# Optimization experiments

Measured on AMD Instinct MI355X. Metric: run time of the kernel, lower is better.

The kernel has to match this reference:

```python
import jax, jax.numpy as jnp
import numpy as np

B, S, D, H = 2, 1024, 2048, 16
NOPE, ROPE, VD, KVR, QLR = 128, 64, 128, 512, 1536
NE, TOPK, MI, SMI = 16, 2, 1408, 2816
QKD = NOPE + ROPE
SCALE = QKD ** -0.5
EPS = 1e-3


def _rms(x, w):
    return w * (x * jax.lax.rsqrt(jnp.mean(x * x, axis=-1, keepdims=True) + EPS))


def _lin(x, w, b):
    return x @ w.T + b


def _rope(x, cos, sin):
    # x: (B,S,H,dr); cos/sin: (S, dr//2); consecutive-pair complex rotation as in torch view_as_complex
    xs = x.reshape(*x.shape[:-1], -1, 2)
    x0, x1 = xs[..., 0], xs[..., 1]
    c = cos[None, :, None, :]
    s = sin[None, :, None, :]
    y = jnp.stack([x0 * c - x1 * s, x0 * s + x1 * c], axis=-1)
    return y.reshape(x.shape)


def setup_inputs() -> dict:
    ks = iter(jax.random.split(jax.random.key(0), 64))

    def w(*shape):
        return jax.random.normal(next(ks), shape, jnp.float32) * 0.02

    ang = jnp.arange(S)[:, None] * (1.0 / (10000.0 ** (jnp.arange(0, ROPE, 2) / ROPE)))[None, :]
    return {
        "x": jax.random.normal(next(ks), (B, S, D), jnp.float32),
        "attn_norm_w": jnp.ones(D, jnp.float32),
        "ffn_norm_w": jnp.ones(D, jnp.float32),
        "wq_a_w": w(QLR, D), "wq_a_b": w(QLR),
        "q_norm_w": jnp.ones(QLR, jnp.float32),
        "wq_b_w": w(H * QKD, QLR), "wq_b_b": w(H * QKD),
        "wkv_a_w": w(KVR + ROPE, D), "wkv_a_b": w(KVR + ROPE),
        "kv_norm_w": jnp.ones(KVR, jnp.float32),
        "wkv_b_w": w(H * (NOPE + VD), KVR),
        "wo_w": w(D, H * VD), "wo_b": w(D),
        "gate_w": w(NE, D), "gate_b": w(NE),
        "e_w1": w(NE, MI, D), "e_b1": w(NE, MI),
        "e_w2": w(NE, D, MI), "e_b2": w(NE, D),
        "e_w3": w(NE, MI, D), "e_b3": w(NE, MI),
        "s_w1": w(SMI, D), "s_b1": w(SMI),
        "s_w2": w(D, SMI), "s_b2": w(D),
        "s_w3": w(SMI, D), "s_b3": w(SMI),
        "cos": jnp.cos(ang), "sin": jnp.sin(ang),
        "start_pos": 0,
    }


def _forward(x, attn_norm_w, ffn_norm_w, wq_a_w, wq_a_b, q_norm_w, wq_b_w, wq_b_b,
             wkv_a_w, wkv_a_b, kv_norm_w, wkv_b_w, wo_w, wo_b,
             gate_w, gate_b, e_w1, e_b1, e_w2, e_b2, e_w3, e_b3,
             s_w1, s_b1, s_w2, s_b2, s_w3, s_b3, cos, sin, start_pos):
    # ---------------- MLA attention ----------------
    h = _rms(x, attn_norm_w)
    q = _lin(_rms(_lin(h, wq_a_w, wq_a_b), q_norm_w), wq_b_w, wq_b_b).reshape(B, S, H, QKD)
    q_nope, q_pe = q[..., :NOPE], q[..., NOPE:]
    q_pe = _rope(q_pe, cos, sin)
    kvf = _lin(h, wkv_a_w, wkv_a_b)
    kv, k_pe = kvf[..., :KVR], kvf[..., KVR:]
    k_pe = _rope(k_pe[:, :, None, :], cos, sin)[:, :, 0, :]          # (B,S,ROPE)
    wb = wkv_b_w.reshape(H, NOPE + VD, KVR)
    q_abs = jnp.einsum('bshd,hdc->bshc', q_nope, wb[:, :NOPE])       # absorbed q (B,S,H,KVR)
    kv_n = _rms(kv, kv_norm_w)                                       # kv cache content, start_pos=0
    scores = (jnp.einsum('bshc,btc->bsht', q_abs, kv_n)
              + jnp.einsum('bshr,btr->bsht', q_pe, k_pe)) * SCALE
    # NOTE: source constructs a causal mask but never applies it -> full attention (faithful)
    p = jax.nn.softmax(scores.astype(jnp.float32), axis=-1).astype(x.dtype)
    o = jnp.einsum('bsht,btc->bshc', p, kv_n)
    o = jnp.einsum('bshc,hdc->bshd', o, wb[:, NOPE:])
    x = x + _lin(o.reshape(B, S, H * VD), wo_w, wo_b)
    # ---------------- MoE FFN ----------------
    h2 = _rms(x, ffn_norm_w).reshape(-1, D)                          # (T,D)
    probs = jax.nn.softmax((h2 @ gate_w.T + gate_b).astype(jnp.float32), axis=-1)
    _, idx = jax.lax.top_k(probs + gate_b, TOPK)                     # bias re-added post-softmax, as in source
    wts = jnp.take_along_axis(probs, idx, axis=-1).astype(x.dtype)   # route_scale = 1.0
    T = h2.shape[0]
    combine = jnp.zeros((T, NE), x.dtype).at[jnp.arange(T)[:, None], idx].add(wts)
    a = jnp.einsum('td,eid->tei', h2, e_w1) + e_b1
    g = jax.nn.silu(a) * (jnp.einsum('td,eid->tei', h2, e_w3) + e_b3)
    gm = g * combine[:, :, None]
    y = jnp.einsum('tei,edi->td', gm, e_w2) + combine @ e_b2
    z = _lin(jax.nn.silu(_lin(h2, s_w1, s_b1)) * _lin(h2, s_w3, s_b3), s_w2, s_b2)
    return x + (y + z + h2).reshape(B, S, D)


def reference(x, attn_norm_w, ffn_norm_w, wq_a_w, wq_a_b, q_norm_w, wq_b_w, wq_b_b,
              wkv_a_w, wkv_a_b, kv_norm_w, wkv_b_w, wo_w, wo_b,
              gate_w, gate_b, e_w1, e_b1, e_w2, e_b2, e_w3, e_b3,
              s_w1, s_b1, s_w2, s_b2, s_w3, s_b3, cos, sin, start_pos):
    return _forward(x, attn_norm_w, ffn_norm_w, wq_a_w, wq_a_b, q_norm_w, wq_b_w, wq_b_b,
                    wkv_a_w, wkv_a_b, kv_norm_w, wkv_b_w, wo_w, wo_b,
                    gate_w, gate_b, e_w1, e_b1, e_w2, e_b2, e_w3, e_b3,
                    s_w1, s_b1, s_w2, s_b2, s_w3, s_b3, cos, sin, start_pos)
```

## Files before the change

kernel.cpp:

```cpp
#include <hip/hip_runtime.h>
#include <math.h>

constexpr int B_ = 2, S_ = 1024, D_ = 2048, H_ = 16;
constexpr int NOPE_ = 128, ROPE_ = 64, VD_ = 128, KVR_ = 512, QLR_ = 1536;
constexpr int NE_ = 16, MI_ = 1408, SMI_ = 2816;
constexpr int QKD_ = NOPE_ + ROPE_;
constexpr int T_ = B_ * S_;
constexpr float SCALE_ = 0.07216878364870322f;
constexpr float EPS_ = 1e-3f;
constexpr int MAX_TILES_ = 80;

typedef __attribute__((ext_vector_type(8))) short  bf16x8_t;
typedef __attribute__((ext_vector_type(4))) float  f32x4_t;
typedef __attribute__((ext_vector_type(4))) unsigned short us4_t;

__device__ __forceinline__ void split_bf(float v, unsigned short& h, unsigned short& l)
{
    unsigned int u = __float_as_uint(v);
    h = (unsigned short)(u >> 16);
    float lo = v - __uint_as_float(u & 0xFFFF0000u);
    l = (unsigned short)(__float_as_uint(lo) >> 16);
}

__device__ __forceinline__ void split4(const float4& v, us4_t& h, us4_t& l)
{
    split_bf(v.x, ((unsigned short*)&h)[0], ((unsigned short*)&l)[0]);
    split_bf(v.y, ((unsigned short*)&h)[1], ((unsigned short*)&l)[1]);
    split_bf(v.z, ((unsigned short*)&h)[2], ((unsigned short*)&l)[2]);
    split_bf(v.w, ((unsigned short*)&h)[3], ((unsigned short*)&l)[3]);
}

__device__ __forceinline__ void stage_rows(
    const float* __restrict__ P, int ldp, int row0, int rowclamp,
    int kt, int sr, int scol,
    unsigned short (*__restrict__ Hs)[40], unsigned short (*__restrict__ Ls)[40])
{
    #pragma unroll
    for (int rr = 0; rr < 128; rr += 32) {
        int row = row0 + rr + sr;
        if (row > rowclamp) row = rowclamp;
        const float4 v = *(const float4*)(P + (long)row * ldp + (kt + scol));
        us4_t h, l;
        split4(v, h, l);
        *(us4_t*)&Hs[rr + sr][scol] = h;
        *(us4_t*)&Ls[rr + sr][scol] = l;
    }
}

__global__ __launch_bounds__(256) void gemm_mfma_kernel(
    const float* __restrict__ A, int lda, long strideA,
    const float* __restrict__ W, int ldw, long strideW, int w_kn,
    const float* __restrict__ A2, int lda2, long strideA2,
    const float* __restrict__ W2, int ldw2, long strideW2, int K2,
    const float* __restrict__ bias, long strideBias,
    const float* __restrict__ res, int ldr, long strideRes, int res_mode,
    float* __restrict__ C, int ldc, long strideC,
    int Nlim, int K)
{
    const int bz = blockIdx.z;
    A += (long)bz * strideA;
    W += (long)bz * strideW;
    C += (long)bz * strideC;
    if (A2)   A2  += (long)bz * strideA2;
    if (W2)   W2  += (long)bz * strideW2;
    if (bias) bias += (long)bz * strideBias;
    if (res)  res  += (long)bz * strideRes;

    __shared__ unsigned short Ah[128][40], Al[128][40];
    __shared__ unsigned short Bh[128][40], Bl[128][40];

    const int m0 = blockIdx.y * 128;
    const int n0 = blockIdx.x * 128;
    const int tid  = threadIdx.x;
    const int lane = tid & 63;
    const int wv   = tid >> 6;
    const int wm = (wv >> 1) * 64, wn = (wv & 1) * 64;
    const int r16 = lane & 15, g4 = lane >> 4;

    f32x4_t acc[4][4];
    #pragma unroll
    for (int i = 0; i < 4; i++)
        #pragma unroll
        for (int j = 0; j < 4; j++) acc[i][j] = (f32x4_t){0.f, 0.f, 0.f, 0.f};

    const int sr   = tid >> 3;
    const int scol = (tid & 7) * 4;
    const int tcol = tid & 63, tkr = tid >> 6;

    for (int kt = 0; kt < K; kt += 32) {
        stage_rows(A, lda, m0, 1 << 30, kt, sr, scol, Ah, Al);
        if (w_kn == 0) {
            stage_rows(W, ldw, n0, Nlim - 1, kt, sr, scol, Bh, Bl);
        } else {
            #pragma unroll
            for (int cb = 0; cb < 128; cb += 64)
                #pragma unroll
                for (int kb = 0; kb < 32; kb += 4) {
                    float v = W[(long)(kt + kb + tkr) * ldw + (n0 + cb + tcol)];
                    unsigned short h, l;
                    split_bf(v, h, l);
                    Bh[cb + tcol][kb + tkr] = h;
                    Bl[cb + tcol][kb + tkr] = l;
                }
        }
        __syncthreads();

        bf16x8_t ah[4], al[4], bh[4], bl[4];
        #pragma unroll
        for (int i = 0; i < 4; i++) {
            ah[i] = *(const bf16x8_t*)&Ah[wm + i * 16 + r16][g4 * 8];
            al[i] = *(const bf16x8_t*)&Al[wm + i * 16 + r16][g4 * 8];
            bh[i] = *(const bf16x8_t*)&Bh[wn + i * 16 + r16][g4 * 8];
            bl[i] = *(const bf16x8_t*)&Bl[wn + i * 16 + r16][g4 * 8];
        }
        #pragma unroll
        for (int i = 0; i < 4; i++)
            #pragma unroll
            for (int j = 0; j < 4; j++) {
                f32x4_t t = acc[i][j];
                t = __builtin_amdgcn_mfma_f32_16x16x32_bf16(ah[i], bh[j], t, 0, 0, 0);
                t = __builtin_amdgcn_mfma_f32_16x16x32_bf16(ah[i], bl[j], t, 0, 0, 0);
                t = __builtin_amdgcn_mfma_f32_16x16x32_bf16(al[i], bh[j], t, 0, 0, 0);
                acc[i][j] = t;
            }
        __syncthreads();
    }

    if (K2 > 0) {
        for (int kt = 0; kt < K2; kt += 32) {
            stage_rows(A2, lda2, m0, 1 << 30, kt, sr, scol, Ah, Al);
            stage_rows(W2, ldw2, n0, Nlim - 1, kt, sr, scol, Bh, Bl);
            __syncthreads();
            bf16x8_t ah[4], al[4], bh[4], bl[4];
            #pragma unroll
            for (int i = 0; i < 4; i++) {
                ah[i] = *(const bf16x8_t*)&Ah[wm + i * 16 + r16][g4 * 8];
                al[i] = *(const bf16x8_t*)&Al[wm + i * 16 + r16][g4 * 8];
                bh[i] = *(const bf16x8_t*)&Bh[wn + i * 16 + r16][g4 * 8];
                bl[i] = *(const bf16x8_t*)&Bl[wn + i * 16 + r16][g4 * 8];
            }
            #pragma unroll
            for (int i = 0; i < 4; i++)
                #pragma unroll
                for (int j = 0; j < 4; j++) {
                    f32x4_t t = acc[i][j];
                    t = __builtin_amdgcn_mfma_f32_16x16x32_bf16(ah[i], bh[j], t, 0, 0, 0);
                    t = __builtin_amdgcn_mfma_f32_16x16x32_bf16(ah[i], bl[j], t, 0, 0, 0);
                    t = __builtin_amdgcn_mfma_f32_16x16x32_bf16(al[i], bh[j], t, 0, 0, 0);
                    acc[i][j] = t;
                }
            __syncthreads();
        }
    }

    #pragma unroll
    for (int i = 0; i < 4; i++)
        #pragma unroll
        for (int rr = 0; rr < 4; rr++) {
            const int m = m0 + wm + i * 16 + g4 * 4 + rr;
            #pragma unroll
            for (int j = 0; j < 4; j++) {
                const int n = n0 + wn + j * 16 + r16;
                if (n >= Nlim) continue;
                float v = acc[i][j][rr];
                if (bias) v += bias[n];
                if (res_mode == 1) {
                    v += res[(long)m * ldr + n];
                } else if (res_mode == 2) {
                    float r = res[(long)m * ldr + n];
                    v = (r / (1.f + expf(-r))) * v;
                }
                C[(long)m * ldc + n] = v;
            }
        }
}

__global__ __launch_bounds__(256) void rms_kernel(
    const float* __restrict__ in, float* __restrict__ out,
    const float* __restrict__ w, int N, int in_stride, int out_stride)
{
    const int row = blockIdx.x;
    const float* x = in + (long)row * in_stride;
    float* y = out + (long)row * out_stride;
    __shared__ float red[256];
    const int tid = threadIdx.x;
    float s = 0.f;
    for (int i = tid; i < N; i += 256) { float v = x[i]; s += v * v; }
    red[tid] = s; __syncthreads();
    for (int st = 128; st > 0; st >>= 1) {
        if (tid < st) red[tid] += red[tid + st];
        __syncthreads();
    }
    const float scale = rsqrtf(red[0] / (float)N + EPS_);
    for (int i = tid; i < N; i += 256) y[i] = w[i] * x[i] * scale;
}

__global__ void rope_kernel(float* __restrict__ p,
                            const float* __restrict__ cosb,
                            const float* __restrict__ sinb,
                            int nheads, int row_stride, int head_stride,
                            int off, int total)
{
    int i = blockIdx.x * 256 + threadIdx.x;
    if (i >= total) return;
    int pair = i & 31;
    int rem = i >> 5;
    int h = rem % nheads;
    int t = rem / nheads;
    int s = t % S_;
    float c = cosb[s * 32 + pair], sn = sinb[s * 32 + pair];
    float* base = p + (long)t * row_stride + (long)h * head_stride + off + pair * 2;
    float x0 = base[0], x1 = base[1];
    base[0] = x0 * c - x1 * sn;
    base[1] = x0 * sn + x1 * c;
}

__global__ __launch_bounds__(256) void softmax_kernel(float* __restrict__ sc)
{
    float* row = sc + (long)blockIdx.x * 1024;
    const int tid = threadIdx.x;
    __shared__ float red[256];

    float4 v = ((const float4*)row)[tid];
    v.x *= SCALE_; v.y *= SCALE_; v.z *= SCALE_; v.w *= SCALE_;

    float m = fmaxf(fmaxf(v.x, v.y), fmaxf(v.z, v.w));
    red[tid] = m; __syncthreads();
    for (int st = 128; st > 0; st >>= 1) {
        if (tid < st) red[tid] = fmaxf(red[tid], red[tid + st]);
        __syncthreads();
    }
    m = red[0];
    __syncthreads();

    v.x = __expf(v.x - m); v.y = __expf(v.y - m);
    v.z = __expf(v.z - m); v.w = __expf(v.w - m);
    float s = v.x + v.y + v.z + v.w;
    red[tid] = s; __syncthreads();
    for (int st = 128; st > 0; st >>= 1) {
        if (tid < st) red[tid] += red[tid + st];
        __syncthreads();
    }
    const float inv = 1.f / red[0];

    v.x *= inv; v.y *= inv; v.z *= inv; v.w *= inv;
    ((float4*)row)[tid] = v;
}

__global__ __launch_bounds__(256) void gate_kernel(
    const float* __restrict__ h2, const float* __restrict__ gw,
    const float* __restrict__ gb, int* __restrict__ idx,
    float* __restrict__ wts)
{
    const int t = blockIdx.x;
    __shared__ float red[256];
    __shared__ float logits[16];
    const int tid = threadIdx.x;
    const int e = tid >> 4, lane = tid & 15;
    const float* x = h2 + (long)t * 2048;
    float s = 0.f;
    for (int i = lane; i < 2048; i += 16) s += x[i] * gw[e * 2048 + i];
    red[tid] = s; __syncthreads();
    for (int st = 8; st > 0; st >>= 1) {
        if (lane < st) red[tid] += red[tid + st];
        __syncthreads();
    }
    if (lane == 0) logits[e] = red[e * 16] + gb[e];
    __syncthreads();
    if (tid == 0) {
        float m = logits[0];
        for (int j = 1; j < 16; j++) m = fmaxf(m, logits[j]);
        float pr[16]; float sum = 0.f;
        for (int j = 0; j < 16; j++) { pr[j] = expf(logits[j] - m); sum += pr[j]; }
        float inv = 1.f / sum;
        for (int j = 0; j < 16; j++) pr[j] *= inv;
        int i1 = 0; float v1 = -1e30f;
        for (int j = 0; j < 16; j++) { float v = pr[j] + gb[j]; if (v > v1) { v1 = v; i1 = j; } }
        int i2 = 0; float v2 = -1e30f;
        for (int j = 0; j < 16; j++) { if (j == i1) continue; float v = pr[j] + gb[j]; if (v > v2) { v2 = v; i2 = j; } }
        idx[t * 2 + 0] = i1; idx[t * 2 + 1] = i2;
        wts[t * 2 + 0] = pr[i1]; wts[t * 2 + 1] = pr[i2];
    }
}

__global__ __launch_bounds__(256) void route_kernel(
    const int* __restrict__ idx, const float* __restrict__ wts,
    int* __restrict__ slot_te, float* __restrict__ slot_w,
    int* __restrict__ tile_e, int* __restrict__ tile_row0,
    int* __restrict__ tile_cnt, int* __restrict__ n_tiles)
{
    __shared__ int counts[16], offs[16], cursor[16];
    const int tid = threadIdx.x;
    if (tid < 16) { counts[tid] = 0; cursor[tid] = 0; }
    __syncthreads();
    for (int a = tid; a < 2 * T_; a += 256) atomicAdd(&counts[idx[a]], 1);
    __syncthreads();
    if (tid == 0) {
        int o = 0;
        for (int e = 0; e < 16; e++) { offs[e] = o; o += counts[e]; }
        int nt = 0;
        for (int e = 0; e < 16; e++) {
            for (int r0 = 0; r0 < counts[e]; r0 += 64) {
                tile_e[nt] = e;
                tile_row0[nt] = offs[e] + r0;
                int c = counts[e] - r0;
                tile_cnt[nt] = c < 64 ? c : 64;
                nt++;
            }
        }
        *n_tiles = nt;
    }
    __syncthreads();
    for (int a = tid; a < 2 * T_; a += 256) {
        int e = idx[a];
        int pos = offs[e] + atomicAdd(&cursor[e], 1);
        int t = a >> 1, k = a & 1;
        slot_te[pos * 2 + 0] = (t << 1) | k;
        slot_te[pos * 2 + 1] = e;
        slot_w[pos] = wts[a];
    }
}

__global__ __launch_bounds__(256) void moe_mlp13_kernel(
    const float* __restrict__ h2,
    const int* __restrict__ slot_te,
    const int* __restrict__ tile_e, const int* __restrict__ tile_row0,
    const int* __restrict__ tile_cnt, const int* __restrict__ n_tiles,
    const float* __restrict__ w1, const float* __restrict__ b1,
    const float* __restrict__ w3, const float* __restrict__ b3,
    float* __restrict__ G)
{
    const int tile = blockIdx.y;
    if (tile >= *n_tiles) return;
    const int e    = tile_e[tile];
    const int row0 = tile_row0[tile];
    const int tcnt = tile_cnt[tile];
    const int n0   = blockIdx.x * 128;

    __shared__ unsigned short Ah[64][40],  Al[64][40];
    __shared__ unsigned short B1h[128][40], B1l[128][40];
    __shared__ unsigned short B3h[128][40], B3l[128][40];
    __shared__ int tok[64];

    const int tid  = threadIdx.x;
    const int lane = tid & 63;
    const int wv   = tid >> 6;
    const int r16 = lane & 15, g4 = lane >> 4;

    if (tid < 64) {
        int r = tid < tcnt ? tid : tcnt - 1;
        tok[tid] = slot_te[(row0 + r) * 2 + 0] >> 1;
    }
    __syncthreads();

    const float* W1 = w1 + (long)e * MI_ * 2048;
    const float* W3 = w3 + (long)e * MI_ * 2048;

    f32x4_t acc1[4][2], acc3[4][2];
    #pragma unroll
    for (int i = 0; i < 4; i++)
        #pragma unroll
        for (int j = 0; j < 2; j++) {
            acc1[i][j] = (f32x4_t){0.f, 0.f, 0.f, 0.f};
            acc3[i][j] = (f32x4_t){0.f, 0.f, 0.f, 0.f};
        }

    const int sr   = tid >> 3;
    const int scol = (tid & 7) * 4;

    for (int kt = 0; kt < 2048; kt += 32) {
        #pragma unroll
        for (int rr = 0; rr < 64; rr += 32) {
            const float4 v = *(const float4*)(h2 + (long)tok[rr + sr] * 2048 + (kt + scol));
            us4_t h, l;
            split4(v, h, l);
            *(us4_t*)&Ah[rr + sr][scol] = h;
            *(us4_t*)&Al[rr + sr][scol] = l;
        }
        #pragma unroll
        for (int rr = 0; rr < 128; rr += 32) {
            const long woff = (long)(n0 + rr + sr) * 2048 + (kt + scol);
            {
                const float4 v = *(const float4*)(W1 + woff);
                us4_t h, l;
                split4(v, h, l);
                *(us4_t*)&B1h[rr + sr][scol] = h;
                *(us4_t*)&B1l[rr + sr][scol] = l;
            }
            {
                const float4 v = *(const float4*)(W3 + woff);
                us4_t h, l;
                split4(v, h, l);
                *(us4_t*)&B3h[rr + sr][scol] = h;
                *(us4_t*)&B3l[rr + sr][scol] = l;
            }
        }
        __syncthreads();

        bf16x8_t ah[4], al[4], b1h[2], b1l[2], b3h[2], b3l[2];
        #pragma unroll
        for (int i = 0; i < 4; i++) {
            ah[i] = *(const bf16x8_t*)&Ah[i * 16 + r16][g4 * 8];
            al[i] = *(const bf16x8_t*)&Al[i * 16 + r16][g4 * 8];
        }
        #pragma unroll
        for (int j = 0; j < 2; j++) {
            const int cn = wv * 32 + j * 16 + r16;
            b1h[j] = *(const bf16x8_t*)&B1h[cn][g4 * 8];
            b1l[j] = *(const bf16x8_t*)&B1l[cn][g4 * 8];
            b3h[j] = *(const bf16x8_t*)&B3h[cn][g4 * 8];
            b3l[j] = *(const bf16x8_t*)&B3l[cn][g4 * 8];
        }
        #pragma unroll
        for (int i = 0; i < 4; i++)
            #pragma unroll
            for (int j = 0; j < 2; j++) {
                f32x4_t t = acc1[i][j];
                t = __builtin_amdgcn_mfma_f32_16x16x32_bf16(ah[i], b1h[j], t, 0, 0, 0);
                t = __builtin_amdgcn_mfma_f32_16x16x32_bf16(ah[i], b1l[j], t, 0, 0, 0);
                t = __builtin_amdgcn_mfma_f32_16x16x32_bf16(al[i], b1h[j], t, 0, 0, 0);
                acc1[i][j] = t;
                f32x4_t u = acc3[i][j];
                u = __builtin_amdgcn_mfma_f32_16x16x32_bf16(ah[i], b3h[j], u, 0, 0, 0);
                u = __builtin_amdgcn_mfma_f32_16x16x32_bf16(ah[i], b3l[j], u, 0, 0, 0);
                u = __builtin_amdgcn_mfma_f32_16x16x32_bf16(al[i], b3h[j], u, 0, 0, 0);
                acc3[i][j] = u;
            }
        __syncthreads();
    }

    #pragma unroll
    for (int i = 0; i < 4; i++)
        #pragma unroll
        for (int rr = 0; rr < 4; rr++) {
            const int rl = i * 16 + g4 * 4 + rr;
            if (rl >= tcnt) continue;
            const long grow = (long)(row0 + rl) * MI_;
            #pragma unroll
            for (int j = 0; j < 2; j++) {
                const int n = n0 + wv * 32 + j * 16 + r16;
                float a = acc1[i][j][rr] + b1[e * MI_ + n];
                float b = acc3[i][j][rr] + b3[e * MI_ + n];
                G[grow + n] = (a / (1.f + expf(-a))) * b;
            }
        }
}

__global__ __launch_bounds__(256) void moe_mlp2_kernel(
    const float* __restrict__ G,
    const int* __restrict__ slot_te, const float* __restrict__ slot_w,
    const int* __restrict__ tile_e, const int* __restrict__ tile_row0,
    const int* __restrict__ tile_cnt, const int* __restrict__ n_tiles,
    const float* __restrict__ w2, const float* __restrict__ b2,
    float* __restrict__ y0, float* __restrict__ y1)
{
    const int tile = blockIdx.y;
    if (tile >= *n_tiles) return;
    const int e    = tile_e[tile];
    const int row0 = tile_row0[tile];
    const int tcnt = tile_cnt[tile];
    const int n0   = blockIdx.x * 128;

    __shared__ unsigned short Ah[64][40], Al[64][40];
    __shared__ unsigned short Bh[128][40], Bl[128][40];
    __shared__ int rsrc[64];

    const int tid  = threadIdx.x;
    const int lane = tid & 63;
    const int wv   = tid >> 6;
    const int r16 = lane & 15, g4 = lane >> 4;

    if (tid < 64) {
        int r = tid < tcnt ? tid : tcnt - 1;
        rsrc[tid] = row0 + r;
    }
    __syncthreads();

    const float* W2 = w2 + (long)e * 2048 * MI_;

    f32x4_t acc[4][2];
    #pragma unroll
    for (int i = 0; i < 4; i++)
        #pragma unroll
        for (int j = 0; j < 2; j++) acc[i][j] = (f32x4_t){0.f, 0.f, 0.f, 0.f};

    const int sr   = tid >> 3;
    const int scol = (tid & 7) * 4;

    for (int kt = 0; kt < MI_; kt += 32) {
        #pragma unroll
        for (int rr = 0; rr < 64; rr += 32) {
            const float4 v = *(const float4*)(G + (long)rsrc[rr + sr] * MI_ + (kt + scol));
            us4_t h, l;
            split4(v, h, l);
            *(us4_t*)&Ah[rr + sr][scol] = h;
            *(us4_t*)&Al[rr + sr][scol] = l;
        }
        #pragma unroll
        for (int rr = 0; rr < 128; rr += 32) {
            const float4 v = *(const float4*)(W2 + (long)(n0 + rr + sr) * MI_ + (kt + scol));
            us4_t h, l;
            split4(v, h, l);
            *(us4_t*)&Bh[rr + sr][scol] = h;
            *(us4_t*)&Bl[rr + sr][scol] = l;
        }
        __syncthreads();

        bf16x8_t ah[4], al[4], bh[2], bl[2];
        #pragma unroll
        for (int i = 0; i < 4; i++) {
            ah[i] = *(const bf16x8_t*)&Ah[i * 16 + r16][g4 * 8];
            al[i] = *(const bf16x8_t*)&Al[i * 16 + r16][g4 * 8];
        }
        #pragma unroll
        for (int j = 0; j < 2; j++) {
            const int cn = wv * 32 + j * 16 + r16;
            bh[j] = *(const bf16x8_t*)&Bh[cn][g4 * 8];
            bl[j] = *(const bf16x8_t*)&Bl[cn][g4 * 8];
        }
        #pragma unroll
        for (int i = 0; i < 4; i++)
            #pragma unroll
            for (int j = 0; j < 2; j++) {
                f32x4_t t = acc[i][j];
                t = __builtin_amdgcn_mfma_f32_16x16x32_bf16(ah[i], bh[j], t, 0, 0, 0);
                t = __builtin_amdgcn_mfma_f32_16x16x32_bf16(ah[i], bl[j], t, 0, 0, 0);
                t = __builtin_amdgcn_mfma_f32_16x16x32_bf16(al[i], bh[j], t, 0, 0, 0);
                acc[i][j] = t;
            }
        __syncthreads();
    }

    #pragma unroll
    for (int i = 0; i < 4; i++)
        #pragma unroll
        for (int rr = 0; rr < 4; rr++) {
            const int rl = i * 16 + g4 * 4 + rr;
            if (rl >= tcnt) continue;
            const int slot = row0 + rl;
            const int tk = slot_te[slot * 2 + 0];
            const int t = tk >> 1, k = tk & 1;
            const float wgt = slot_w[slot];
            float* y = (k ? y1 : y0) + (long)t * 2048;
            #pragma unroll
            for (int j = 0; j < 2; j++) {
                const int n = n0 + wv * 32 + j * 16 + r16;
                y[n] = wgt * (acc[i][j][rr] + b2[e * 2048 + n]);
            }
        }
}

__global__ void final_add_kernel(const float* __restrict__ x2,
                                 const float* __restrict__ h2,
                                 const float* __restrict__ y0,
                                 const float* __restrict__ y1,
                                 const float* __restrict__ z,
                                 float* __restrict__ out, long n)
{
    long i = (long)blockIdx.x * 256 + threadIdx.x;
    if (i >= n) return;
    out[i] = x2[i] + h2[i] + y0[i] + y1[i] + z[i];
}

extern "C" void kernel_launch(void* const* d_in, const int* in_sizes, int n_in,
                              void* d_out, int out_size, void* d_ws, size_t ws_size,
                              hipStream_t stream)
{
    (void)in_sizes; (void)n_in; (void)out_size; (void)ws_size;

    const float* x          = (const float*)d_in[0];
    const float* attn_nw    = (const float*)d_in[1];
    const float* ffn_nw     = (const float*)d_in[2];
    const float* wq_a_w     = (const float*)d_in[3];
    const float* wq_a_b     = (const float*)d_in[4];
    const float* q_norm_w   = (const float*)d_in[5];
    const float* wq_b_w     = (const float*)d_in[6];
    const float* wq_b_b     = (const float*)d_in[7];
    const float* wkv_a_w    = (const float*)d_in[8];
    const float* wkv_a_b    = (const float*)d_in[9];
    const float* kv_norm_w  = (const float*)d_in[10];
    const float* wkv_b_w    = (const float*)d_in[11];
    const float* wo_w       = (const float*)d_in[12];
    const float* wo_b       = (const float*)d_in[13];
    const float* gate_w     = (const float*)d_in[14];
    const float* gate_b     = (const float*)d_in[15];
    const float* e_w1       = (const float*)d_in[16];
    const float* e_b1       = (const float*)d_in[17];
    const float* e_w2       = (const float*)d_in[18];
    const float* e_b2       = (const float*)d_in[19];
    const float* e_w3       = (const float*)d_in[20];
    const float* e_b3       = (const float*)d_in[21];
    const float* s_w1       = (const float*)d_in[22];
    const float* s_b1       = (const float*)d_in[23];
    const float* s_w2       = (const float*)d_in[24];
    const float* s_b2       = (const float*)d_in[25];
    const float* s_w3       = (const float*)d_in[26];
    const float* s_b3       = (const float*)d_in[27];
    const float* cosb       = (const float*)d_in[28];
    const float* sinb       = (const float*)d_in[29];

    float* ws = (float*)d_ws;
    float* h    = ws + 0;
    float* qa   = ws + 4194304;
    float* q    = ws + 7340032;
    float* kvf  = ws + 13631488;
    float* qabs = ws + 14811136;
    float* o2   = ws + 31588352;
    float* x2   = ws + 35782656;
    float* h2   = ws + 39976960;
    float* u1   = ws + 44171264;
    float* u3   = ws + 49938432;
    float* wts  = ws + 55705600;
    int*   idx  = (int*)(ws + 55709696);
    int*   slot_te = (int*)(ws + 55713792);
    float* slot_w  = ws + 55721984;
    float* y0 = h;
    float* y1 = q;
    float* z  = u3;

    float* scores = o2;

    float* G = qabs;
    int* tile_e    = (int*)(qabs + 5767168);
    int* tile_row0 = tile_e + MAX_TILES_;
    int* tile_cnt  = tile_e + 2 * MAX_TILES_;
    int* n_tiles   = tile_e + 3 * MAX_TILES_;

    rms_kernel<<<dim3(T_), 256, 0, stream>>>(x, h, attn_nw, 2048, 2048, 2048);

    gemm_mfma_kernel<<<dim3(QLR_ / 128, T_ / 128, 1), 256, 0, stream>>>(
        h, 2048, 0, wq_a_w, 2048, 0, 0,
        nullptr, 0, 0, nullptr, 0, 0, 0,
        wq_a_b, 0, nullptr, 0, 0, 0,
        qa, QLR_, 0, QLR_, 2048);

    rms_kernel<<<dim3(T_), 256, 0, stream>>>(qa, qa, q_norm_w, QLR_, QLR_, QLR_);

    gemm_mfma_kernel<<<dim3(H_ * QKD_ / 128, T_ / 128, 1), 256, 0, stream>>>(
        qa, QLR_, 0, wq_b_w, QLR_, 0, 0,
        nullptr, 0, 0, nullptr, 0, 0, 0,
        wq_b_b, 0, nullptr, 0, 0, 0,
        q, H_ * QKD_, 0, H_ * QKD_, QLR_);

    gemm_mfma_kernel<<<dim3(5, T_ / 128, 1), 256, 0, stream>>>(
        h, 2048, 0, wkv_a_w, 2048, 0, 0,
        nullptr, 0, 0, nullptr, 0, 0, 0,
        wkv_a_b, 0, nullptr, 0, 0, 0,
        kvf, KVR_ + ROPE_, 0, KVR_ + ROPE_, 2048);

    {
        int total_q = T_ * H_ * 32;
        rope_kernel<<<dim3((total_q + 255) / 256), 256, 0, stream>>>(
            q, cosb, sinb, H_, H_ * QKD_, QKD_, NOPE_, total_q);
        int total_k = T_ * 32;
        rope_kernel<<<dim3((total_k + 255) / 256), 256, 0, stream>>>(
            kvf, cosb, sinb, 1, KVR_ + ROPE_, 0, KVR_, total_k);
    }

    rms_kernel<<<dim3(T_), 256, 0, stream>>>(kvf, kvf, kv_norm_w, KVR_,
                                             KVR_ + ROPE_, KVR_ + ROPE_);

    gemm_mfma_kernel<<<dim3(KVR_ / 128, T_ / 128, H_), 256, 0, stream>>>(
        q, H_ * QKD_, QKD_,
        wkv_b_w, KVR_, (long)256 * KVR_, 1,
        nullptr, 0, 0, nullptr, 0, 0, 0,
        nullptr, 0, nullptr, 0, 0, 0,
        qabs, H_ * KVR_, KVR_, KVR_, NOPE_);

    for (int b = 0; b < B_; b++) {
        const float* kvb = kvf + (long)b * S_ * (KVR_ + ROPE_);
        gemm_mfma_kernel<<<dim3(S_ / 128, S_ / 128, H_), 256, 0, stream>>>(
            qabs + (long)b * S_ * H_ * KVR_, H_ * KVR_, KVR_,
            kvb, KVR_ + ROPE_, 0, 0,
            q + (long)b * S_ * H_ * QKD_ + NOPE_, H_ * QKD_, QKD_,
            kvb + KVR_, KVR_ + ROPE_, 0, ROPE_,
            nullptr, 0, nullptr, 0, 0, 0,
            scores, S_, (long)S_ * S_, S_, KVR_);
        softmax_kernel<<<dim3(H_ * S_), 256, 0, stream>>>(scores);
        gemm_mfma_kernel<<<dim3(KVR_ / 128, S_ / 128, H_), 256, 0, stream>>>(
            scores, S_, (long)S_ * S_,
            kvb, KVR_ + ROPE_, 0, 1,
            nullptr, 0, 0, nullptr, 0, 0, 0,
            nullptr, 0, nullptr, 0, 0, 0,
            qabs + (long)b * S_ * H_ * KVR_, H_ * KVR_, KVR_, KVR_, S_);
    }

    gemm_mfma_kernel<<<dim3(VD_ / 128, T_ / 128, H_), 256, 0, stream>>>(
        qabs, H_ * KVR_, KVR_,
        wkv_b_w + (long)NOPE_ * KVR_, KVR_, (long)256 * KVR_, 0,
        nullptr, 0, 0, nullptr, 0, 0, 0,
        nullptr, 0, nullptr, 0, 0, 0,
        o2, H_ * VD_, VD_, VD_, KVR_);

    gemm_mfma_kernel<<<dim3(D_ / 128, T_ / 128, 1), 256, 0, stream>>>(
        o2, 2048, 0, wo_w, 2048, 0, 0,
        nullptr, 0, 0, nullptr, 0, 0, 0,
        wo_b, 0, x, 2048, 0, 1,
        x2, 2048, 0, D_, 2048);

    rms_kernel<<<dim3(T_), 256, 0, stream>>>(x2, h2, ffn_nw, 2048, 2048, 2048);

    gate_kernel<<<dim3(T_), 256, 0, stream>>>(h2, gate_w, gate_b, idx, wts);

    route_kernel<<<dim3(1), 256, 0, stream>>>(idx, wts, slot_te, slot_w,
                                              tile_e, tile_row0, tile_cnt, n_tiles);

    moe_mlp13_kernel<<<dim3(MI_ / 128, MAX_TILES_), 256, 0, stream>>>(
        h2, slot_te, tile_e, tile_row0, tile_cnt, n_tiles,
        e_w1, e_b1, e_w3, e_b3, G);
    moe_mlp2_kernel<<<dim3(D_ / 128, MAX_TILES_), 256, 0, stream>>>(
        G, slot_te, slot_w, tile_e, tile_row0, tile_cnt, n_tiles,
        e_w2, e_b2, y0, y1);

    gemm_mfma_kernel<<<dim3(SMI_ / 128, T_ / 128, 1), 256, 0, stream>>>(
        h2, 2048, 0, s_w1, 2048, 0, 0,
        nullptr, 0, 0, nullptr, 0, 0, 0,
        s_b1, 0, nullptr, 0, 0, 0,
        u1, SMI_, 0, SMI_, 2048);
    gemm_mfma_kernel<<<dim3(SMI_ / 128, T_ / 128, 1), 256, 0, stream>>>(
        h2, 2048, 0, s_w3, 2048, 0, 0,
        nullptr, 0, 0, nullptr, 0, 0, 0,
        s_b3, 0, u1, SMI_, 0, 2,
        u1, SMI_, 0, SMI_, 2048);
    gemm_mfma_kernel<<<dim3(D_ / 128, T_ / 128, 1), 256, 0, stream>>>(
        u1, SMI_, 0, s_w2, SMI_, 0, 0,
        nullptr, 0, 0, nullptr, 0, 0, 0,
        s_b2, 0, nullptr, 0, 0, 0,
        z, D_, 0, D_, SMI_);

    {
        long n = (long)T_ * D_;
        final_add_kernel<<<dim3((unsigned)((n + 255) / 256)), 256, 0, stream>>>(
            x2, h2, y0, y1, z, (float*)d_out, n);
    }
}
```

Before: 2.684 ms.

## Pre-split operands into bf16 hi/lo planes and stage GEMM tiles via direct-to-LDS loads

Rewrites the dense GEMM to read pre-split bf16 hi/lo plane buffers instead of fp32, moving the split out of the inner loop into separate conversion kernels and producer epilogues (RMS, softmax, GEMM outputs). Tiles are now staged with global_load_lds into XOR-swizzled 64-wide K tiles, and transposed plane copies of wkv_b and kvf remove the strided k-major path. This cuts per-tile conversion work and halves bytes read per element, at the cost of extra conversion kernels run every call and more intermediate memory traffic.

Result: faster. 2.210 ms (-17.6%).

```diff
diff --git a/kernel.cpp b/kernel.cpp
--- a/kernel.cpp
+++ b/kernel.cpp
@@ -10,70 +10,79 @@
 constexpr float EPS_ = 1e-3f;
 constexpr int MAX_TILES_ = 80;
 
+typedef unsigned short u16;
 typedef __attribute__((ext_vector_type(8))) short  bf16x8_t;
 typedef __attribute__((ext_vector_type(4))) float  f32x4_t;
-typedef __attribute__((ext_vector_type(4))) unsigned short us4_t;
-
-__device__ __forceinline__ void split_bf(float v, unsigned short& h, unsigned short& l)
+typedef __attribute__((ext_vector_type(4))) u16 us4_t;
+
+constexpr long E_H = 4194304, E_QA = 3145728, E_Q = 6291456, E_KVF = 1179648;
+constexpr long E_KVFT = 1048576, E_QABS = 16777216, E_SCORES = 16777216;
+constexpr long E_O2 = 4194304, E_H2 = 4194304, E_U1 = 5767168, E_G = 5767168;
+constexpr long E_WQA = 3145728, E_WQB = 4718592, E_WKVA = 1310720;
+constexpr long E_WKVB = 2097152, E_WKVB1T = 1048576, E_WO = 4194304, E_SW = 5767168;
+
+__device__ __forceinline__ void split_bf(float v, u16& h, u16& l)
 {
     unsigned int u = __float_as_uint(v);
-    h = (unsigned short)(u >> 16);
+    h = (u16)(u >> 16);
     float lo = v - __uint_as_float(u & 0xFFFF0000u);
-    l = (unsigned short)(__float_as_uint(lo) >> 16);
+    l = (u16)(__float_as_uint(lo) >> 16);
 }
 
 __device__ __forceinline__ void split4(const float4& v, us4_t& h, us4_t& l)
 {
-    split_bf(v.x, ((unsigned short*)&h)[0], ((unsigned short*)&l)[0]);
-    split_bf(v.y, ((unsigned short*)&h)[1], ((unsigned short*)&l)[1]);
-    split_bf(v.z, ((unsigned short*)&h)[2], ((unsigned short*)&l)[2]);
-    split_bf(v.w, ((unsigned short*)&h)[3], ((unsigned short*)&l)[3]);
-}
-
-__device__ __forceinline__ void stage_rows(
-    const float* __restrict__ P, int ldp, int row0, int rowclamp,
-    int kt, int sr, int scol,
-    unsigned short (*__restrict__ Hs)[40], unsigned short (*__restrict__ Ls)[40])
-{
-    #pragma unroll
-    for (int rr = 0; rr < 128; rr += 32) {
-        int row = row0 + rr + sr;
-        if (row > rowclamp) row = rowclamp;
-        const float4 v = *(const float4*)(P + (long)row * ldp + (kt + scol));
-        us4_t h, l;
-        split4(v, h, l);
-        *(us4_t*)&Hs[rr + sr][scol] = h;
-        *(us4_t*)&Ls[rr + sr][scol] = l;
-    }
-}
-
-__global__ __launch_bounds__(256) void gemm_mfma_kernel(
-    const float* __restrict__ A, int lda, long strideA,
-    const float* __restrict__ W, int ldw, long strideW, int w_kn,
-    const float* __restrict__ A2, int lda2, long strideA2,
-    const float* __restrict__ W2, int ldw2, long strideW2, int K2,
-    const float* __restrict__ bias, long strideBias,
+    split_bf(v.x, ((u16*)&h)[0], ((u16*)&l)[0]);
+    split_bf(v.y, ((u16*)&h)[1], ((u16*)&l)[1]);
+    split_bf(v.z, ((u16*)&h)[2], ((u16*)&l)[2]);
+    split_bf(v.w, ((u16*)&h)[3], ((u16*)&l)[3]);
+}
+
+__device__ __forceinline__ void stage_one(
+    const u16* __restrict__ g, int ld, int kt, u16* lds, int lane, int wv)
+{
+    #pragma unroll
+    for (int it = 0; it < 4; it++) {
+        const int issue = wv * 4 + it;
+        const int row = issue * 8 + (lane >> 3);
+        const int colb = ((lane & 7) << 4) ^ ((row & 7) << 4);
+        const u16* gp = g + (long)row * ld + kt + (colb >> 1);
+        u16* lp = lds + issue * 512;
+        __builtin_amdgcn_global_load_lds(
+            (const __attribute__((address_space(1))) unsigned int*)gp,
+            (__attribute__((address_space(3))) unsigned int*)lp, 16, 0, 0);
+    }
+}
+
+__device__ __forceinline__ bf16x8_t fragld(const u16* lds, int row, int slot)
+{
+    const int byte = (row << 7) + ((slot << 4) ^ ((row & 7) << 4));
+    return *(const bf16x8_t*)((const char*)lds + byte);
+}
+
+__global__ __launch_bounds__(256) void gemm_bf_kernel(
+    const u16* __restrict__ A, long ploA, int lda, long strideA,
+    const u16* __restrict__ B, long ploB, int ldb, long strideB,
+    const u16* __restrict__ A2, long ploA2, int lda2, long strideA2,
+    const u16* __restrict__ B2, long ploB2, int ldb2, long strideB2, int K2,
+    const float* __restrict__ bias,
     const float* __restrict__ res, int ldr, long strideRes, int res_mode,
-    float* __restrict__ C, int ldc, long strideC,
+    float* __restrict__ Cf, u16* __restrict__ Cp, long ploC,
+    int ldc, long strideC,
     int Nlim, int K)
 {
     const int bz = blockIdx.z;
-    A += (long)bz * strideA;
-    W += (long)bz * strideW;
-    C += (long)bz * strideC;
-    if (A2)   A2  += (long)bz * strideA2;
-    if (W2)   W2  += (long)bz * strideW2;
-    if (bias) bias += (long)bz * strideBias;
-    if (res)  res  += (long)bz * strideRes;
-
-    __shared__ unsigned short Ah[128][40], Al[128][40];
-    __shared__ unsigned short Bh[128][40], Bl[128][40];
-
-    const int m0 = blockIdx.y * 128;
-    const int n0 = blockIdx.x * 128;
-    const int tid  = threadIdx.x;
-    const int lane = tid & 63;
-    const int wv   = tid >> 6;
+    A += bz * strideA; B += bz * strideB;
+    if (A2)  A2 += bz * strideA2;
+    if (B2)  B2 += bz * strideB2;
+    if (res) res += bz * strideRes;
+    if (Cf)  Cf += bz * strideC;
+    if (Cp)  Cp += bz * strideC;
+
+    __shared__ __align__(16) u16 Ah[128 * 64], Al[128 * 64];
+    __shared__ __align__(16) u16 Bh[128 * 64], Bl[128 * 64];
+
+    const int m0 = blockIdx.y * 128, n0 = blockIdx.x * 128;
+    const int tid = threadIdx.x, lane = tid & 63, wv = tid >> 6;
     const int wm = (wv >> 1) * 64, wn = (wv & 1) * 64;
     const int r16 = lane & 15, g4 = lane >> 4;
 
@@ -83,61 +92,17 @@
         #pragma unroll
         for (int j = 0; j < 4; j++) acc[i][j] = (f32x4_t){0.f, 0.f, 0.f, 0.f};
 
-    const int sr   = tid >> 3;
-    const int scol = (tid & 7) * 4;
-    const int tcol = tid & 63, tkr = tid >> 6;
-
-    for (int kt = 0; kt < K; kt += 32) {
-        stage_rows(A, lda, m0, 1 << 30, kt, sr, scol, Ah, Al);
-        if (w_kn == 0) {
-            stage_rows(W, ldw, n0, Nlim - 1, kt, sr, scol, Bh, Bl);
-        } else {
-            #pragma unroll
-            for (int cb = 0; cb < 128; cb += 64)
-                #pragma unroll
-                for (int kb = 0; kb < 32; kb += 4) {
-                    float v = W[(long)(kt + kb + tkr) * ldw + (n0 + cb + tcol)];
-                    unsigned short h, l;
-                    split_bf(v, h, l);
-                    Bh[cb + tcol][kb + tkr] = h;
-                    Bl[cb + tcol][kb + tkr] = l;
-                }
-        }
-        __syncthreads();
-
-        bf16x8_t ah[4], al[4], bh[4], bl[4];
-        #pragma unroll
-        for (int i = 0; i < 4; i++) {
-            ah[i] = *(const bf16x8_t*)&Ah[wm + i * 16 + r16][g4 * 8];
-            al[i] = *(const bf16x8_t*)&Al[wm + i * 16 + r16][g4 * 8];
-            bh[i] = *(const bf16x8_t*)&Bh[wn + i * 16 + r16][g4 * 8];
-            bl[i] = *(const bf16x8_t*)&Bl[wn + i * 16 + r16][g4 * 8];
-        }
-        #pragma unroll
-        for (int i = 0; i < 4; i++)
-            #pragma unroll
-            for (int j = 0; j < 4; j++) {
-                f32x4_t t = acc[i][j];
-                t = __builtin_amdgcn_mfma_f32_16x16x32_bf16(ah[i], bh[j], t, 0, 0, 0);
-                t = __builtin_amdgcn_mfma_f32_16x16x32_bf16(ah[i], bl[j], t, 0, 0, 0);
-                t = __builtin_amdgcn_mfma_f32_16x16x32_bf16(al[i], bh[j], t, 0, 0, 0);
-                acc[i][j] = t;
-            }
-        __syncthreads();
-    }
-
-    if (K2 > 0) {
-        for (int kt = 0; kt < K2; kt += 32) {
-            stage_rows(A2, lda2, m0, 1 << 30, kt, sr, scol, Ah, Al);
-            stage_rows(W2, ldw2, n0, Nlim - 1, kt, sr, scol, Bh, Bl);
-            __syncthreads();
+    auto do_tile = [&]() {
+        #pragma unroll
+        for (int ks = 0; ks < 2; ks++) {
+            const int slot = ks * 4 + g4;
             bf16x8_t ah[4], al[4], bh[4], bl[4];
             #pragma unroll
             for (int i = 0; i < 4; i++) {
-                ah[i] = *(const bf16x8_t*)&Ah[wm + i * 16 + r16][g4 * 8];
-                al[i] = *(const bf16x8_t*)&Al[wm + i * 16 + r16][g4 * 8];
-                bh[i] = *(const bf16x8_t*)&Bh[wn + i * 16 + r16][g4 * 8];
-                bl[i] = *(const bf16x8_t*)&Bl[wn + i * 16 + r16][g4 * 8];
+                ah[i] = fragld(Ah, wm + i * 16 + r16, slot);
+                al[i] = fragld(Al, wm + i * 16 + r16, slot);
+                bh[i] = fragld(Bh, wn + i * 16 + r16, slot);
+                bl[i] = fragld(Bl, wn + i * 16 + r16, slot);
             }
             #pragma unroll
             for (int i = 0; i < 4; i++)
@@ -149,6 +114,30 @@
                     t = __builtin_amdgcn_mfma_f32_16x16x32_bf16(al[i], bh[j], t, 0, 0, 0);
                     acc[i][j] = t;
                 }
+        }
+    };
+
+    const u16* Ab = A + (long)m0 * lda;
+    const u16* Bb = B + (long)n0 * ldb;
+    for (int kt = 0; kt < K; kt += 64) {
+        stage_one(Ab,        lda, kt, Ah, lane, wv);
+        stage_one(Ab + ploA, lda, kt, Al, lane, wv);
+        stage_one(Bb,        ldb, kt, Bh, lane, wv);
+        stage_one(Bb + ploB, ldb, kt, Bl, lane, wv);
+        __syncthreads();
+        do_tile();
+        __syncthreads();
+    }
+    if (K2 > 0) {
+        const u16* A2b = A2 + (long)m0 * lda2;
+        const u16* B2b = B2 + (long)n0 * ldb2;
+        for (int kt = 0; kt < K2; kt += 64) {
+            stage_one(A2b,         lda2, kt, Ah, lane, wv);
+            stage_one(A2b + ploA2, lda2, kt, Al, lane, wv);
+            stage_one(B2b,         ldb2, kt, Bh, lane, wv);
+            stage_one(B2b + ploB2, ldb2, kt, Bl, lane, wv);
+            __syncthreads();
+            do_tile();
             __syncthreads();
         }
     }
@@ -170,9 +159,96 @@
                     float r = res[(long)m * ldr + n];
                     v = (r / (1.f + expf(-r))) * v;
                 }
-                C[(long)m * ldc + n] = v;
+                if (Cf) {
+                    Cf[(long)m * ldc + n] = v;
+                } else {
+                    u16 hh, ll; split_bf(v, hh, ll);
+                    Cp[(long)m * ldc + n] = hh;
+                    Cp[ploC + (long)m * ldc + n] = ll;
+                }
             }
         }
+}
+
+__global__ void conv_pl_kernel(const float* __restrict__ src,
+                               u16* __restrict__ dst, long plo, long n)
+{
+    long i = ((long)blockIdx.x * 256 + threadIdx.x) * 4;
+    if (i >= n) return;
+    float4 v = *(const float4*)(src + i);
+    us4_t h, l; split4(v, h, l);
+    *(us4_t*)(dst + i) = h;
+    *(us4_t*)(dst + plo + i) = l;
+}
+
+__global__ __launch_bounds__(256) void conv_wkvb1T_kernel(
+    const float* __restrict__ src, u16* __restrict__ dst, long plo)
+{
+    __shared__ float t[32][33];
+    const int h = blockIdx.z, n0 = blockIdx.y * 32, k0 = blockIdx.x * 32;
+    const int tx = threadIdx.x & 31, ty = threadIdx.x >> 5;
+    #pragma unroll
+    for (int i = 0; i < 4; i++) {
+        int k = k0 + ty + i * 8;
+        t[ty + i * 8][tx] = src[((long)(h * 256 + k)) * 512 + (n0 + tx)];
+    }
+    __syncthreads();
+    #pragma unroll
+    for (int i = 0; i < 4; i++) {
+        int n = n0 + ty + i * 8;
+        float v = t[tx][ty + i * 8];
+        u16 hh, ll; split_bf(v, hh, ll);
+        long o = ((long)h * 512 + n) * 128 + (k0 + tx);
+        dst[o] = hh; dst[plo + o] = ll;
+    }
+}
+
+__global__ __launch_bounds__(256) void conv_kvfT_kernel(
+    const float* __restrict__ src, u16* __restrict__ dst, long plo)
+{
+    __shared__ float tl[32][33];
+    const int b = blockIdx.z, c0 = blockIdx.y * 32, t0 = blockIdx.x * 32;
+    const int tx = threadIdx.x & 31, ty = threadIdx.x >> 5;
+    #pragma unroll
+    for (int i = 0; i < 4; i++) {
+        int t = t0 + ty + i * 8;
+        tl[ty + i * 8][tx] = src[((long)(b * 1024 + t)) * 576 + (c0 + tx)];
+    }
+    __syncthreads();
+    #pragma unroll
+    for (int i = 0; i < 4; i++) {
+        int c = c0 + ty + i * 8;
+        float v = tl[tx][ty + i * 8];
+        u16 hh, ll; split_bf(v, hh, ll);
+        long o = ((long)b * 512 + c) * 1024 + (t0 + tx);
+        dst[o] = hh; dst[plo + o] = ll;
+    }
+}
+
+__global__ __launch_bounds__(256) void rms_pl_kernel(
+    const float* __restrict__ in, int in_stride,
+    u16* __restrict__ outp, long plo, int out_stride,
+    const float* __restrict__ w, int N, float* __restrict__ outf)
+{
+    const int row = blockIdx.x;
+    const float* x = in + (long)row * in_stride;
+    __shared__ float red[256];
+    const int tid = threadIdx.x;
+    float s = 0.f;
+    for (int i = tid; i < N; i += 256) { float v = x[i]; s += v * v; }
+    red[tid] = s; __syncthreads();
+    for (int st = 128; st > 0; st >>= 1) {
+        if (tid < st) red[tid] += red[tid + st];
+        __syncthreads();
+    }
+    const float scale = rsqrtf(red[0] / (float)N + EPS_);
+    for (int i = tid; i < N; i += 256) {
+        float v = w[i] * x[i] * scale;
+        u16 hh, ll; split_bf(v, hh, ll);
+        outp[(long)row * out_stride + i] = hh;
+        outp[plo + (long)row * out_stride + i] = ll;
+        if (outf) outf[(long)row * out_stride + i] = v;
+    }
 }
 
 __global__ __launch_bounds__(256) void rms_kernel(
@@ -215,13 +291,15 @@
     base[1] = x0 * sn + x1 * c;
 }
 
-__global__ __launch_bounds__(256) void softmax_kernel(float* __restrict__ sc)
-{
-    float* row = sc + (long)blockIdx.x * 1024;
+__global__ __launch_bounds__(256) void softmax_pl_kernel(
+    const float* __restrict__ in, u16* __restrict__ outp, long plo)
+{
+    const long row = blockIdx.x;
+    const float* src = in + row * 1024;
     const int tid = threadIdx.x;
     __shared__ float red[256];
 
-    float4 v = ((const float4*)row)[tid];
+    float4 v = ((const float4*)src)[tid];
     v.x *= SCALE_; v.y *= SCALE_; v.z *= SCALE_; v.w *= SCALE_;
 
     float m = fmaxf(fmaxf(v.x, v.y), fmaxf(v.z, v.w));
@@ -242,9 +320,11 @@
         __syncthreads();
     }
     const float inv = 1.f / red[0];
-
     v.x *= inv; v.y *= inv; v.z *= inv; v.w *= inv;
-    ((float4*)row)[tid] = v;
+
+    us4_t h, l; split4(v, h, l);
+    *(us4_t*)(outp + row * 1024 + tid * 4) = h;
+    *(us4_t*)(outp + plo + row * 1024 + tid * 4) = l;
 }
 
 __global__ __launch_bounds__(256) void gate_kernel(
@@ -322,13 +402,13 @@
 }
 
 __global__ __launch_bounds__(256) void moe_mlp13_kernel(
-    const float* __restrict__ h2,
+    const u16* __restrict__ h2p, long ploH2,
     const int* __restrict__ slot_te,
     const int* __restrict__ tile_e, const int* __restrict__ tile_row0,
     const int* __restrict__ tile_cnt, const int* __restrict__ n_tiles,
     const float* __restrict__ w1, const float* __restrict__ b1,
     const float* __restrict__ w3, const float* __restrict__ b3,
-    float* __restrict__ G)
+    u16* __restrict__ Gp, long ploG)
 {
     const int tile = blockIdx.y;
     if (tile >= *n_tiles) return;
@@ -337,9 +417,9 @@
     const int tcnt = tile_cnt[tile];
     const int n0   = blockIdx.x * 128;
 
-    __shared__ unsigned short Ah[64][40],  Al[64][40];
-    __shared__ unsigned short B1h[128][40], B1l[128][40];
-    __shared__ unsigned short B3h[128][40], B3l[128][40];
+    __shared__ u16 Ah[64][40],  Al[64][40];
+    __shared__ u16 B1h[128][40], B1l[128][40];
+    __shared__ u16 B3h[128][40], B3l[128][40];
     __shared__ int tok[64];
 
     const int tid  = threadIdx.x;
@@ -371,26 +451,22 @@
     for (int kt = 0; kt < 2048; kt += 32) {
         #pragma unroll
         for (int rr = 0; rr < 64; rr += 32) {
-            const float4 v = *(const float4*)(h2 + (long)tok[rr + sr] * 2048 + (kt + scol));
-            us4_t h, l;
-            split4(v, h, l);
-            *(us4_t*)&Ah[rr + sr][scol] = h;
-            *(us4_t*)&Al[rr + sr][scol] = l;
+            long o = (long)tok[rr + sr] * 2048 + (kt + scol);
+            *(us4_t*)&Ah[rr + sr][scol] = *(const us4_t*)(h2p + o);
+            *(us4_t*)&Al[rr + sr][scol] = *(const us4_t*)(h2p + ploH2 + o);
         }
         #pragma unroll
         for (int rr = 0; rr < 128; rr += 32) {
             const long woff = (long)(n0 + rr + sr) * 2048 + (kt + scol);
             {
                 const float4 v = *(const float4*)(W1 + woff);
-                us4_t h, l;
-                split4(v, h, l);
+                us4_t h, l; split4(v, h, l);
                 *(us4_t*)&B1h[rr + sr][scol] = h;
                 *(us4_t*)&B1l[rr + sr][scol] = l;
             }
             {
                 const float4 v = *(const float4*)(W3 + woff);
-                us4_t h, l;
-                split4(v, h, l);
+                us4_t h, l; split4(v, h, l);
                 *(us4_t*)&B3h[rr + sr][scol] = h;
                 *(us4_t*)&B3l[rr + sr][scol] = l;
             }
@@ -441,13 +517,16 @@
                 const int n = n0 + wv * 32 + j * 16 + r16;
                 float a = acc1[i][j][rr] + b1[e * MI_ + n];
                 float b = acc3[i][j][rr] + b3[e * MI_ + n];
-                G[grow + n] = (a / (1.f + expf(-a))) * b;
+                float g = (a / (1.f + expf(-a))) * b;
+                u16 hh, ll; split_bf(g, hh, ll);
+                Gp[grow + n] = hh;
+                Gp[ploG + grow + n] = ll;
             }
         }
 }
 
 __global__ __launch_bounds__(256) void moe_mlp2_kernel(
-    const float* __restrict__ G,
+    const u16* __restrict__ Gp, long ploG,
     const int* __restrict__ slot_te, const float* __restrict__ slot_w,
     const int* __restrict__ tile_e, const int* __restrict__ tile_row0,
     const int* __restrict__ tile_cnt, const int* __restrict__ n_tiles,
@@ -461,8 +540,8 @@
     const int tcnt = tile_cnt[tile];
     const int n0   = blockIdx.x * 128;
 
-    __shared__ unsigned short Ah[64][40], Al[64][40];
-    __shared__ unsigned short Bh[128][40], Bl[128][40];
+    __shared__ u16 Ah[64][40], Al[64][40];
+    __shared__ u16 Bh[128][40], Bl[128][40];
     __shared__ int rsrc[64];
 
     const int tid  = threadIdx.x;
@@ -490,17 +569,14 @@
     for (int kt = 0; kt < MI_; kt += 32) {
         #pragma unroll
         for (int rr = 0; rr < 64; rr += 32) {
-            const float4 v = *(const float4*)(G + (long)rsrc[rr + sr] * MI_ + (kt + scol));
-            us4_t h, l;
-            split4(v, h, l);
-            *(us4_t*)&Ah[rr + sr][scol] = h;
-            *(us4_t*)&Al[rr + sr][scol] = l;
+            long o = (long)rsrc[rr + sr] * MI_ + (kt + scol);
+            *(us4_t*)&Ah[rr + sr][scol] = *(const us4_t*)(Gp + o);
+            *(us4_t*)&Al[rr + sr][scol] = *(const us4_t*)(Gp + ploG + o);
         }
         #pragma unroll
         for (int rr = 0; rr < 128; rr += 32) {
             const float4 v = *(const float4*)(W2 + (long)(n0 + rr + sr) * MI_ + (kt + scol));
-            us4_t h, l;
-            split4(v, h, l);
+            us4_t h, l; split4(v, h, l);
             *(us4_t*)&Bh[rr + sr][scol] = h;
             *(us4_t*)&Bl[rr + sr][scol] = l;
         }
@@ -600,137 +676,163 @@
     const float* sinb       = (const float*)d_in[29];
 
     float* ws = (float*)d_ws;
-    float* h    = ws + 0;
-    float* qa   = ws + 4194304;
-    float* q    = ws + 7340032;
-    float* kvf  = ws + 13631488;
-    float* qabs = ws + 14811136;
-    float* o2   = ws + 31588352;
-    float* x2   = ws + 35782656;
-    float* h2   = ws + 39976960;
-    float* u1   = ws + 44171264;
-    float* u3   = ws + 49938432;
-    float* wts  = ws + 55705600;
-    int*   idx  = (int*)(ws + 55709696);
-    int*   slot_te = (int*)(ws + 55713792);
-    float* slot_w  = ws + 55721984;
-    float* y0 = h;
-    float* y1 = q;
-    float* z  = u3;
-
-    float* scores = o2;
-
-    float* G = qabs;
-    int* tile_e    = (int*)(qabs + 5767168);
-    int* tile_row0 = tile_e + MAX_TILES_;
-    int* tile_cnt  = tile_e + 2 * MAX_TILES_;
-    int* n_tiles   = tile_e + 3 * MAX_TILES_;
-
-    rms_kernel<<<dim3(T_), 256, 0, stream>>>(x, h, attn_nw, 2048, 2048, 2048);
-
-    gemm_mfma_kernel<<<dim3(QLR_ / 128, T_ / 128, 1), 256, 0, stream>>>(
-        h, 2048, 0, wq_a_w, 2048, 0, 0,
-        nullptr, 0, 0, nullptr, 0, 0, 0,
-        wq_a_b, 0, nullptr, 0, 0, 0,
-        qa, QLR_, 0, QLR_, 2048);
-
-    rms_kernel<<<dim3(T_), 256, 0, stream>>>(qa, qa, q_norm_w, QLR_, QLR_, QLR_);
-
-    gemm_mfma_kernel<<<dim3(H_ * QKD_ / 128, T_ / 128, 1), 256, 0, stream>>>(
-        qa, QLR_, 0, wq_b_w, QLR_, 0, 0,
-        nullptr, 0, 0, nullptr, 0, 0, 0,
-        wq_b_b, 0, nullptr, 0, 0, 0,
-        q, H_ * QKD_, 0, H_ * QKD_, QLR_);
-
-    gemm_mfma_kernel<<<dim3(5, T_ / 128, 1), 256, 0, stream>>>(
-        h, 2048, 0, wkv_a_w, 2048, 0, 0,
-        nullptr, 0, 0, nullptr, 0, 0, 0,
-        wkv_a_b, 0, nullptr, 0, 0, 0,
-        kvf, KVR_ + ROPE_, 0, KVR_ + ROPE_, 2048);
+
+    float* qa_f   = ws + 0;
+    float* q_f    = ws + 3145728;
+    float* kvf_f  = ws + 9437184;
+    float* x2     = ws + 10616832;
+    float* h2_f   = ws + 14811136;
+    float* u1_f   = ws + 19005440;
+    float* y0     = ws + 24772608;
+    float* y1     = ws + 28966912;
+    float* z      = ws + 33161216;
+    float* wts    = ws + 37355520;
+    int*   idx    = (int*)(ws + 37359616);
+    int*   slot_te= (int*)(ws + 37363712);
+    float* slot_w = ws + 37371904;
+    int*   tile_e = (int*)(ws + 37376000);
+    int*   tile_row0 = tile_e + MAX_TILES_;
+    int*   tile_cnt  = tile_e + 2 * MAX_TILES_;
+    int*   n_tiles   = tile_e + 3 * MAX_TILES_;
+    float* scores_f = u1_f;
+    u16*   G_pl   = (u16*)(ws + 0);
+
+    u16* h_pl     = (u16*)(ws + 37377024);
+    u16* qa_pl    = (u16*)(ws + 41571328);
+    u16* q_pl     = (u16*)(ws + 44717056);
+    u16* kvf_pl   = (u16*)(ws + 51008512);
+    u16* kvfT_pl  = (u16*)(ws + 52188160);
+    u16* qabs_pl  = (u16*)(ws + 53236736);
+    u16* sc_pl    = (u16*)(ws + 70013952);
+    u16* o2_pl    = (u16*)(ws + 86791168);
+    u16* h2_pl    = (u16*)(ws + 90985472);
+    u16* u1_pl    = (u16*)(ws + 95179776);
+    u16* wqa_pl   = (u16*)(ws + 100946944);
+    u16* wqb_pl   = (u16*)(ws + 104092672);
+    u16* wkva_pl  = (u16*)(ws + 108811264);
+    u16* wkvb_pl  = (u16*)(ws + 110121984);
+    u16* wkvb1T_pl= (u16*)(ws + 112219136);
+    u16* wo_pl    = (u16*)(ws + 113267712);
+    u16* sw1_pl   = (u16*)(ws + 117462016);
+    u16* sw3_pl   = (u16*)(ws + 123229184);
+    u16* sw2_pl   = (u16*)(ws + 128996352);
+
+    conv_pl_kernel<<<dim3(3072), 256, 0, stream>>>(wq_a_w, wqa_pl, E_WQA, 3145728);
+    conv_pl_kernel<<<dim3(4608), 256, 0, stream>>>(wq_b_w, wqb_pl, E_WQB, 4718592);
+    conv_pl_kernel<<<dim3(1152), 256, 0, stream>>>(wkv_a_w, wkva_pl, E_WKVA, 1179648);
+    conv_pl_kernel<<<dim3(2048), 256, 0, stream>>>(wkv_b_w, wkvb_pl, E_WKVB, 2097152);
+    conv_pl_kernel<<<dim3(4096), 256, 0, stream>>>(wo_w, wo_pl, E_WO, 4194304);
+    conv_pl_kernel<<<dim3(5632), 256, 0, stream>>>(s_w1, sw1_pl, E_SW, 5767168);
+    conv_pl_kernel<<<dim3(5632), 256, 0, stream>>>(s_w3, sw3_pl, E_SW, 5767168);
+    conv_pl_kernel<<<dim3(5632), 256, 0, stream>>>(s_w2, sw2_pl, E_SW, 5767168);
+    conv_wkvb1T_kernel<<<dim3(4, 16, 16), 256, 0, stream>>>(wkv_b_w, wkvb1T_pl, E_WKVB1T);
+
+    rms_pl_kernel<<<dim3(T_), 256, 0, stream>>>(x, 2048, h_pl, E_H, 2048, attn_nw, 2048, nullptr);
+
+    gemm_bf_kernel<<<dim3(12, 16, 1), 256, 0, stream>>>(
+        h_pl, E_H, 2048, 0, wqa_pl, E_WQA, 2048, 0,
+        nullptr, 0, 0, 0, nullptr, 0, 0, 0, 0,
+        wq_a_b, nullptr, 0, 0, 0,
+        qa_f, nullptr, 0, QLR_, 0, QLR_, 2048);
+
+    rms_pl_kernel<<<dim3(T_), 256, 0, stream>>>(qa_f, QLR_, qa_pl, E_QA, QLR_, q_norm_w, QLR_, nullptr);
+
+    gemm_bf_kernel<<<dim3(24, 16, 1), 256, 0, stream>>>(
+        qa_pl, E_QA, QLR_, 0, wqb_pl, E_WQB, QLR_, 0,
+        nullptr, 0, 0, 0, nullptr, 0, 0, 0, 0,
+        wq_b_b, nullptr, 0, 0, 0,
+        q_f, nullptr, 0, H_ * QKD_, 0, H_ * QKD_, QLR_);
+
+    gemm_bf_kernel<<<dim3(5, 16, 1), 256, 0, stream>>>(
+        h_pl, E_H, 2048, 0, wkva_pl, E_WKVA, 2048, 0,
+        nullptr, 0, 0, 0, nullptr, 0, 0, 0, 0,
+        wkv_a_b, nullptr, 0, 0, 0,
+        kvf_f, nullptr, 0, KVR_ + ROPE_, 0, KVR_ + ROPE_, 2048);
 
     {
         int total_q = T_ * H_ * 32;
         rope_kernel<<<dim3((total_q + 255) / 256), 256, 0, stream>>>(
-            q, cosb, sinb, H_, H_ * QKD_, QKD_, NOPE_, total_q);
+            q_f, cosb, sinb, H_, H_ * QKD_, QKD_, NOPE_, total_q);
         int total_k = T_ * 32;
         rope_kernel<<<dim3((total_k + 255) / 256), 256, 0, stream>>>(
-            kvf, cosb, sinb, 1, KVR_ + ROPE_, 0, KVR_, total_k);
-    }
-
-    rms_kernel<<<dim3(T_), 256, 0, stream>>>(kvf, kvf, kv_norm_w, KVR_,
+            kvf_f, cosb, sinb, 1, KVR_ + ROPE_, 0, KVR_, total_k);
+    }
+
+    rms_kernel<<<dim3(T_), 256, 0, stream>>>(kvf_f, kvf_f, kv_norm_w, KVR_,
                                              KVR_ + ROPE_, KVR_ + ROPE_);
 
-    gemm_mfma_kernel<<<dim3(KVR_ / 128, T_ / 128, H_), 256, 0, stream>>>(
-        q, H_ * QKD_, QKD_,
-        wkv_b_w, KVR_, (long)256 * KVR_, 1,
-        nullptr, 0, 0, nullptr, 0, 0, 0,
-        nullptr, 0, nullptr, 0, 0, 0,
-        qabs, H_ * KVR_, KVR_, KVR_, NOPE_);
+    conv_pl_kernel<<<dim3(6144), 256, 0, stream>>>(q_f, q_pl, E_Q, 6291456);
+    conv_pl_kernel<<<dim3(1152), 256, 0, stream>>>(kvf_f, kvf_pl, E_KVF, 1179648);
+    conv_kvfT_kernel<<<dim3(32, 16, 2), 256, 0, stream>>>(kvf_f, kvfT_pl, E_KVFT);
+
+    gemm_bf_kernel<<<dim3(4, 16, 16), 256, 0, stream>>>(
+        q_pl, E_Q, H_ * QKD_, 192, wkvb1T_pl, E_WKVB1T, 128, (long)512 * 128,
+        nullptr, 0, 0, 0, nullptr, 0, 0, 0, 0,
+        nullptr, nullptr, 0, 0, 0,
+        nullptr, qabs_pl, E_QABS, H_ * KVR_, KVR_, KVR_, NOPE_);
 
     for (int b = 0; b < B_; b++) {
-        const float* kvb = kvf + (long)b * S_ * (KVR_ + ROPE_);
-        gemm_mfma_kernel<<<dim3(S_ / 128, S_ / 128, H_), 256, 0, stream>>>(
-            qabs + (long)b * S_ * H_ * KVR_, H_ * KVR_, KVR_,
-            kvb, KVR_ + ROPE_, 0, 0,
-            q + (long)b * S_ * H_ * QKD_ + NOPE_, H_ * QKD_, QKD_,
-            kvb + KVR_, KVR_ + ROPE_, 0, ROPE_,
-            nullptr, 0, nullptr, 0, 0, 0,
-            scores, S_, (long)S_ * S_, S_, KVR_);
-        softmax_kernel<<<dim3(H_ * S_), 256, 0, stream>>>(scores);
-        gemm_mfma_kernel<<<dim3(KVR_ / 128, S_ / 128, H_), 256, 0, stream>>>(
-            scores, S_, (long)S_ * S_,
-            kvb, KVR_ + ROPE_, 0, 1,
-            nullptr, 0, 0, nullptr, 0, 0, 0,
-            nullptr, 0, nullptr, 0, 0, 0,
-            qabs + (long)b * S_ * H_ * KVR_, H_ * KVR_, KVR_, KVR_, S_);
-    }
-
-    gemm_mfma_kernel<<<dim3(VD_ / 128, T_ / 128, H_), 256, 0, stream>>>(
-        qabs, H_ * KVR_, KVR_,
-        wkv_b_w + (long)NOPE_ * KVR_, KVR_, (long)256 * KVR_, 0,
-        nullptr, 0, 0, nullptr, 0, 0, 0,
-        nullptr, 0, nullptr, 0, 0, 0,
-        o2, H_ * VD_, VD_, VD_, KVR_);
-
-    gemm_mfma_kernel<<<dim3(D_ / 128, T_ / 128, 1), 256, 0, stream>>>(
-        o2, 2048, 0, wo_w, 2048, 0, 0,
-        nullptr, 0, 0, nullptr, 0, 0, 0,
-        wo_b, 0, x, 2048, 0, 1,
-        x2, 2048, 0, D_, 2048);
-
-    rms_kernel<<<dim3(T_), 256, 0, stream>>>(x2, h2, ffn_nw, 2048, 2048, 2048);
-
-    gate_kernel<<<dim3(T_), 256, 0, stream>>>(h2, gate_w, gate_b, idx, wts);
-
+        gemm_bf_kernel<<<dim3(8, 8, 16), 256, 0, stream>>>(
+            qabs_pl + (long)b * S_ * H_ * KVR_, E_QABS, H_ * KVR_, KVR_,
+            kvf_pl + (long)b * S_ * (KVR_ + ROPE_), E_KVF, KVR_ + ROPE_, 0,
+            q_pl + (long)b * S_ * H_ * QKD_ + NOPE_, E_Q, H_ * QKD_, QKD_,
+            kvf_pl + (long)b * S_ * (KVR_ + ROPE_) + KVR_, E_KVF, KVR_ + ROPE_, 0, ROPE_,
+            nullptr, nullptr, 0, 0, 0,
+            scores_f, nullptr, 0, S_, (long)S_ * S_, S_, KVR_);
+        softmax_pl_kernel<<<dim3(H_ * S_), 256, 0, stream>>>(scores_f, sc_pl, E_SCORES);
+        gemm_bf_kernel<<<dim3(4, 8, 16), 256, 0, stream>>>(
+            sc_pl, E_SCORES, S_, (long)S_ * S_,
+            kvfT_pl + (long)b * KVR_ * S_, E_KVFT, S_, 0,
+            nullptr, 0, 0, 0, nullptr, 0, 0, 0, 0,
+            nullptr, nullptr, 0, 0, 0,
+            nullptr, qabs_pl + (long)b * S_ * H_ * KVR_, E_QABS, H_ * KVR_, KVR_, KVR_, S_);
+    }
+
+    gemm_bf_kernel<<<dim3(1, 16, 16), 256, 0, stream>>>(
+        qabs_pl, E_QABS, H_ * KVR_, KVR_,
+        wkvb_pl + (long)NOPE_ * KVR_, E_WKVB, KVR_, (long)256 * KVR_,
+        nullptr, 0, 0, 0, nullptr, 0, 0, 0, 0,
+        nullptr, nullptr, 0, 0, 0,
+        nullptr, o2_pl, E_O2, H_ * VD_, VD_, VD_, KVR_);
+
+    gemm_bf_kernel<<<dim3(16, 16, 1), 256, 0, stream>>>(
+        o2_pl, E_O2, 2048, 0, wo_pl, E_WO, 2048, 0,
+        nullptr, 0, 0, 0, nullptr, 0, 0, 0, 0,
+        wo_b, x, 2048, 0, 1,
+        x2, nullptr, 0, D_, 0, D_, 2048);
+
+    rms_pl_kernel<<<dim3(T_), 256, 0, stream>>>(x2, 2048, h2_pl, E_H2, 2048, ffn_nw, 2048, h2_f);
+
+    gate_kernel<<<dim3(T_), 256, 0, stream>>>(h2_f, gate_w, gate_b, idx, wts);
     route_kernel<<<dim3(1), 256, 0, stream>>>(idx, wts, slot_te, slot_w,
                                               tile_e, tile_row0, tile_cnt, n_tiles);
 
     moe_mlp13_kernel<<<dim3(MI_ / 128, MAX_TILES_), 256, 0, stream>>>(
-        h2, slot_te, tile_e, tile_row0, tile_cnt, n_tiles,
-        e_w1, e_b1, e_w3, e_b3, G);
+        h2_pl, E_H2, slot_te, tile_e, tile_row0, tile_cnt, n_tiles,
+        e_w1, e_b1, e_w3, e_b3, G_pl, E_G);
     moe_mlp2_kernel<<<dim3(D_ / 128, MAX_TILES_), 256, 0, stream>>>(
-        G, slot_te, slot_w, tile_e, tile_row0, tile_cnt, n_tiles,
+        G_pl, E_G, slot_te, slot_w, tile_e, tile_row0, tile_cnt, n_tiles,
         e_w2, e_b2, y0, y1);
 
-    gemm_mfma_kernel<<<dim3(SMI_ / 128, T_ / 128, 1), 256, 0, stream>>>(
-        h2, 2048, 0, s_w1, 2048, 0, 0,
-        nullptr, 0, 0, nullptr, 0, 0, 0,
-        s_b1, 0, nullptr, 0, 0, 0,
-        u1, SMI_, 0, SMI_, 2048);
-    gemm_mfma_kernel<<<dim3(SMI_ / 128, T_ / 128, 1), 256, 0, stream>>>(
-        h2, 2048, 0, s_w3, 2048, 0, 0,
-        nullptr, 0, 0, nullptr, 0, 0, 0,
-        s_b3, 0, u1, SMI_, 0, 2,
-        u1, SMI_, 0, SMI_, 2048);
-    gemm_mfma_kernel<<<dim3(D_ / 128, T_ / 128, 1), 256, 0, stream>>>(
-        u1, SMI_, 0, s_w2, SMI_, 0, 0,
-        nullptr, 0, 0, nullptr, 0, 0, 0,
-        s_b2, 0, nullptr, 0, 0, 0,
-        z, D_, 0, D_, SMI_);
+    gemm_bf_kernel<<<dim3(22, 16, 1), 256, 0, stream>>>(
+        h2_pl, E_H2, 2048, 0, sw1_pl, E_SW, 2048, 0,
+        nullptr, 0, 0, 0, nullptr, 0, 0, 0, 0,
+        s_b1, nullptr, 0, 0, 0,
+        u1_f, nullptr, 0, SMI_, 0, SMI_, 2048);
+    gemm_bf_kernel<<<dim3(22, 16, 1), 256, 0, stream>>>(
+        h2_pl, E_H2, 2048, 0, sw3_pl, E_SW, 2048, 0,
+        nullptr, 0, 0, 0, nullptr, 0, 0, 0, 0,
+        s_b3, u1_f, SMI_, 0, 2,
+        nullptr, u1_pl, E_U1, SMI_, 0, SMI_, 2048);
+    gemm_bf_kernel<<<dim3(16, 16, 1), 256, 0, stream>>>(
+        u1_pl, E_U1, SMI_, 0, sw2_pl, E_SW, SMI_, 0,
+        nullptr, 0, 0, 0, nullptr, 0, 0, 0, 0,
+        s_b2, nullptr, 0, 0, 0,
+        z, nullptr, 0, D_, 0, D_, SMI_);
 
     {
         long n = (long)T_ * D_;
         final_add_kernel<<<dim3((unsigned)((n + 255) / 256)), 256, 0, stream>>>(
-            x2, h2, y0, y1, z, (float*)d_out, n);
-    }
-}
+            x2, h2_f, y0, y1, z, (float*)d_out, n);
+    }
+}
```
